# Kernel tuning notes

Measured on AMD Instinct MI355X. Metric: run time of the kernel, lower is better.

## Reference

```python
import jax, jax.numpy as jnp
import numpy as np


def _patchify(x, p):
    # x: [B, V, H, W] -> [B, V, L, p*p] with L = (H/p)*(W/p), matching Conv2d(kernel=stride=p)
    B, V, H, W = x.shape
    hp, wp = H // p, W // p
    x = x.reshape(B, V, hp, p, wp, p)
    x = x.transpose(0, 1, 2, 4, 3, 5)  # [B, V, hp, wp, p, p]
    return x.reshape(B, V, hp * wp, p * p)


def setup_inputs() -> dict:
    key = jax.random.key(0)
    ks = jax.random.split(key, 12)
    B, V, H, W, p, D = 2, 16, 128, 256, 4, 1024
    L = (H // p) * (W // p)  # 2048
    std = 0.02
    return {
        "x": jax.random.normal(ks[0], (B, V, H, W), jnp.float32),
        "proj_w": jax.random.normal(ks[1], (V, D, p * p), jnp.float32) * std,
        "proj_b": jnp.zeros((V, D), jnp.float32),
        "channel_embed": jax.random.normal(ks[2], (1, V, D), jnp.float32) * std,
        "pos_embed": jax.random.normal(ks[3], (1, L, D), jnp.float32) * std,
        "channel_query": jax.random.normal(ks[4], (1, 1, D), jnp.float32) * std,
        "wq": jax.random.normal(ks[5], (D, D), jnp.float32) * std,
        "wk": jax.random.normal(ks[6], (D, D), jnp.float32) * std,
        "wv": jax.random.normal(ks[7], (D, D), jnp.float32) * std,
        "bq": jnp.zeros((D,), jnp.float32),
        "bk": jnp.zeros((D,), jnp.float32),
        "bv": jnp.zeros((D,), jnp.float32),
        "wo": jax.random.normal(ks[8], (D, D), jnp.float32) * std,
        "bo": jnp.zeros((D,), jnp.float32),
        "num_heads": 16,
    }


def reference(x, proj_w, proj_b, channel_embed, pos_embed, channel_query,
              wq, wk, wv, bq, bk, bv, wo, bo, num_heads):
    D = proj_w.shape[1]
    p = int(round(np.sqrt(proj_w.shape[-1])))
    nh = int(num_heads)
    dh = D // nh

    # per-variable patch embed (Conv2d k=stride=p == patch-matmul)
    patches = _patchify(x, p)                                   # [B, V, L, p*p]
    tok = jnp.einsum('bvlk,vdk->bvld', patches, proj_w)         # [B, V, L, D]
    tok = tok + proj_b[None, :, None, :]

    # add variable (channel) and positional embeddings
    tok = tok + channel_embed[:, :, None, :] + pos_embed[:, None, :, :]

    # aggregate_variables: single-query MHA over V, batched over B*L
    h = tok.transpose(0, 2, 1, 3)                               # [B, L, V, D]
    q = channel_query[0, 0] @ wq.T + bq                         # [D]
    qh = q.reshape(nh, dh)
    k = (jnp.einsum('blvd,ed->blve', h, wk) + bk).reshape(*h.shape[:3], nh, dh)
    v = (jnp.einsum('blvd,ed->blve', h, wv) + bv).reshape(*h.shape[:3], nh, dh)
    scores = jnp.einsum('he,blvhe->blhv', qh, k) / np.sqrt(dh)  # [B, L, nh, V]
    attn = jax.nn.softmax(scores, axis=-1)
    ctx = jnp.einsum('blhv,blvhe->blhe', attn, v)               # [B, L, nh, dh]
    ctx = ctx.reshape(h.shape[0], h.shape[1], D)
    out = ctx @ wo.T + bo                                       # [B, L, D]
    return out
```

## Files before the change

kernel.cpp:

```cpp
#include <hip/hip_runtime.h>
#include <hip/hip_bf16.h>

using bf16 = __hip_bfloat16;
using bf16x8 = __attribute__((ext_vector_type(8))) short;
using f32x4  = __attribute__((ext_vector_type(4))) float;

__device__ inline unsigned short f2bu(float f){ bf16 h = __float2bfloat16(f); return *(unsigned short*)&h; }
__device__ inline void async_cp16(const void* g, void* l){
  __builtin_amdgcn_global_load_lds((const __attribute__((address_space(1))) void*)g,
                                   (__attribute__((address_space(3))) void*)l, 16, 0, 0);
}
union BF8 { unsigned short s[8]; bf16x8 v; };

constexpr int D_ = 1024, L_ = 2048;
constexpr int CN = 384;

__device__ inline size_t w3idx(int row, int col){
  const int hh = row >> 6, m = row & 15, dt = (row >> 4) & 3;
  const int vp = col >> 5, quad = (col >> 3) & 3, j = col & 7;
  return (size_t)hh*18432 + vp*2048 + dt*512 + quad*128 + m*8 + j;
}

__global__ __launch_bounds__(256) void k_prep2(const float* __restrict__ wv, const float* __restrict__ wo,
                                               const float* __restrict__ pe,
                                               const float* __restrict__ proj_w, const float* __restrict__ proj_b,
                                               const float* __restrict__ ce, const float* __restrict__ cq,
                                               const float* __restrict__ wq, const float* __restrict__ bq,
                                               const float* __restrict__ wk,
                                               unsigned short* __restrict__ Ab, unsigned short* __restrict__ wo_b,
                                               unsigned short* __restrict__ pe_b,
                                               unsigned short* __restrict__ Btb){
  __shared__ float t[64][17];
  __shared__ float qL[64];
  __shared__ float red[4][64];
  const int blk = blockIdx.x;
  const int tid = threadIdx.x;
  if (blk < 4096){
    int i = blk*256 + tid;
    const float* src; unsigned short* dst; size_t off;
    if (i < 262144){ src = wv; dst = Ab;   off = i; }
    else if (i < 524288){ src = wo; dst = wo_b; off = i - 262144; }
    else           { src = pe; dst = pe_b; off = i - 524288; }
    float4 v = *(const float4*)(src + off*4);
    *(ushort4*)(dst + off*4) = make_ushort4(f2bu(v.x), f2bu(v.y), f2bu(v.z), f2bu(v.w));
  } else if (blk < 4352){
    const int r_ = blk - 4096;
    const int v = r_ >> 4, dd0 = (r_ & 15)*64;
    { const int r = tid >> 2, kq = tid & 3;
      float4 a = *(const float4*)(proj_w + ((size_t)(v*D_ + dd0 + r))*16 + kq*4);
      t[r][kq*4+0]=a.x; t[r][kq*4+1]=a.y; t[r][kq*4+2]=a.z; t[r][kq*4+3]=a.w; }
    __syncthreads();
    { const int k = tid >> 4, c0 = (tid & 15)*4;
      ushort4 o = make_ushort4(f2bu(t[c0+0][k]), f2bu(t[c0+1][k]), f2bu(t[c0+2][k]), f2bu(t[c0+3][k]));
      *(ushort4*)(Btb + (size_t)(v*16+k)*D_ + dd0 + c0) = o; }
    if (tid < 16){
      const int c0 = tid*4;
      float4 pb = *(const float4*)(proj_b + v*D_ + dd0 + c0);
      float4 cc = *(const float4*)(ce     + v*D_ + dd0 + c0);
      ushort4 o = make_ushort4(f2bu(pb.x+cc.x), f2bu(pb.y+cc.y), f2bu(pb.z+cc.z), f2bu(pb.w+cc.w));
      *(ushort4*)(Btb + (size_t)(256+v)*D_ + dd0 + c0) = o;
    }
  } else {
    const int b = blk - 4352;
    const int hh = b >> 4, dq = b & 15;
    const int wave = tid >> 6, lane = tid & 63;
    {
      float cqv[16];
      #pragma unroll
      for (int k=0;k<16;++k) cqv[k] = cq[lane + 64*k];
      #pragma unroll
      for (int j=0;j<16;++j){
        const int e = hh*64 + wave*16 + j;
        const float* wr = wq + (size_t)e*D_;
        float p = 0.f;
        #pragma unroll
        for (int k=0;k<16;++k) p += cqv[k]*wr[lane + 64*k];
        #pragma unroll
        for (int m=32;m>=1;m>>=1) p += __shfl_xor(p, m, 64);
        if (lane==0) qL[wave*16+j] = p + bq[e];
      }
    }
    __syncthreads();
    {
      const int eg = wave, dl = lane;
      const int d = dq*64 + dl;
      float s = 0.f;
      #pragma unroll
      for (int j=0;j<16;++j){
        int e = hh*64 + eg*16 + j;
        s += qL[eg*16+j]*wk[(size_t)e*D_ + d];
      }
      red[eg][dl] = s;
      __syncthreads();
      if (eg==0)
        Ab[(size_t)(1024+hh)*D_ + d] = f2bu(((red[0][dl]+red[1][dl]) + (red[2][dl]+red[3][dl]))*0.125f);
    }
  }
}

template<int MFRAG, bool BIAS, bool WB2>
__device__ inline void gemm_body(unsigned short* As, unsigned short* Bs,
                                 const unsigned short* __restrict__ Abf, const unsigned short* __restrict__ Bt,
                                 const float* __restrict__ bias, float* __restrict__ C,
                                 unsigned short* __restrict__ W, const float* __restrict__ bvp,
                                 int m0, int n0, int K, int ldc, int Mvalid){
  const int tid = threadIdx.x;
  const int wave = tid >> 6, lane = tid & 63;
  const int wm = wave & 1, wn = wave >> 1;
  const int lm = lane & 15, kg4 = lane >> 4;
  f32x4 acc[MFRAG][4];
  #pragma unroll
  for (int mf=0;mf<MFRAG;++mf)
    #pragma unroll
    for (int nf=0;nf<4;++nf) acc[mf][nf] = (f32x4){0.f,0.f,0.f,0.f};
  for (int k0=0; k0<K; k0+=64){
    #pragma unroll
    for (int i=0;i<MFRAG;++i){
      int idx = i*256 + tid;
      int row = idx >> 3, g = (idx & 7) ^ (row & 7);
      async_cp16(Abf + (size_t)(m0+row)*K + k0 + g*8, &As[idx*8]);
    }
    #pragma unroll
    for (int i=0;i<4;++i){
      int idx = i*256 + tid;
      int row = idx >> 3, g = (idx & 7) ^ (row & 7);
      async_cp16(Bt + (size_t)(n0+row)*K + k0 + g*8, &Bs[idx*8]);
    }
    __syncthreads();
    #pragma unroll
    for (int c=0;c<2;++c){
      bf16x8 af[MFRAG], bfr[4];
      #pragma unroll
      for (int f=0;f<MFRAG;++f){
        int row = wm*16*MFRAG + f*16 + lm;
        af[f] = *(const bf16x8*)(&As[row*64 + (((c*4+kg4) ^ (row&7)))*8]);
      }
      #pragma unroll
      for (int f=0;f<4;++f){
        int colr = wn*64 + f*16 + lm;
        bfr[f] = *(const bf16x8*)(&Bs[colr*64 + (((c*4+kg4) ^ (colr&7)))*8]);
      }
      #pragma unroll
      for (int mf=0;mf<MFRAG;++mf)
        #pragma unroll
        for (int nf=0;nf<4;++nf)
          acc[mf][nf] = __builtin_amdgcn_mfma_f32_16x16x32_bf16(af[mf], bfr[nf], acc[mf][nf], 0,0,0);
    }
    __syncthreads();
  }
  #pragma unroll
  for (int nf=0;nf<4;++nf){
    int col = n0 + wn*64 + nf*16 + lm;
    float bval = BIAS ? bias[col] : 0.f;
    #pragma unroll
    for (int mf=0;mf<MFRAG;++mf){
      #pragma unroll
      for (int r=0;r<4;++r){
        int row = m0 + wm*16*MFRAG + mf*16 + kg4*4 + r;
        if (row < Mvalid){
          float v = acc[mf][nf][r];
          C[(size_t)row*ldc + col] = v + bval;
          if (WB2 && row < 1024){
            if (col < 256)      W[w3idx(row,col)] = f2bu(v);
            else if (col < 272) W[w3idx(row,col)] = f2bu(v + bvp[row]);
            else if (col < 288) W[w3idx(row,col)] = 0;
          }
        }
      }
    }
  }
}

__global__ __launch_bounds__(256) void k_gemmCP2(const unsigned short* __restrict__ Ab,
                                                 const unsigned short* __restrict__ Btb,
                                                 const unsigned short* __restrict__ pe_b,
                                                 const float* __restrict__ bv,
                                                 float* __restrict__ Cbig, unsigned short* __restrict__ Wb2,
                                                 float* __restrict__ P2){
  __shared__ unsigned short As[64*64];
  __shared__ unsigned short Bs[128*64];
  if (blockIdx.x < 51){
    int bx = blockIdx.x % 3, by = blockIdx.x / 3;
    gemm_body<2,false,true>(As, Bs, Ab, Btb, nullptr, Cbig, Wb2, bv, by*64, bx*128, 1024, CN, 1040);
  } else {
    int b = blockIdx.x - 51;
    int bx = b & 7, by = b >> 3;
    gemm_body<1,false,false>(As, Bs, pe_b, Ab, nullptr, P2, nullptr, nullptr, by*32, bx*128, 1024, 1024, 2048);
  }
}

__global__ __launch_bounds__(256) void k_gemmOut(const unsigned short* __restrict__ ctxF,
                                                 const unsigned short* __restrict__ wo_b,
                                                 const float* __restrict__ bo, float* __restrict__ C){
  __shared__ unsigned short As[64*64];
  __shared__ unsigned short Bs[128*64];
  gemm_body<2,true,false>(As, Bs, ctxF, wo_b, bo, C, nullptr, nullptr,
                          blockIdx.y*64, blockIdx.x*128, 1024, 1024, 4096);
}

__global__ __launch_bounds__(1024) void k_fused10(const float* __restrict__ x,
                                                  const float* __restrict__ Cbig,
                                                  const unsigned short* __restrict__ W3,
                                                  const float* __restrict__ P2,
                                                  unsigned short* __restrict__ ctxF){
  __shared__ float patchP[16*260];
  __shared__ float attnT[16*320];
  __shared__ __align__(16) unsigned short S[16*1032];
  const int tid = threadIdx.x;
  const int bb  = blockIdx.x >> 7;
  const int sg  = blockIdx.x & 127;
  unsigned short* ctx = ctxF + (size_t)bb*L_*D_;
  const int l0 = sg*16;
  {
    const int u = tid & 15, pi = (tid >> 4) & 3, v = tid >> 6;
    const int hi = l0 >> 6, wi0 = l0 & 63;
    const float* xp = x + ((size_t)((bb*16+v)*128 + hi*4 + pi)*256 + (wi0+u)*4);
    float4 r = *(const float4*)xp;
    float* dst = &patchP[u*260 + v*16 + pi*4];
    dst[0]=r.x; dst[1]=r.y; dst[2]=r.z; dst[3]=r.w;
  }
  __syncthreads();
  if (tid < 256){
    const int s = tid >> 4, h = tid & 15;
    const float* qrow = Cbig + (size_t)(1024+h)*CN;
    const float* prow = &patchP[s*260];
    float4 qc0 = *(const float4*)(qrow+256);
    float4 qc1 = *(const float4*)(qrow+260);
    float4 qc2 = *(const float4*)(qrow+264);
    float4 qc3 = *(const float4*)(qrow+268);
    float qcv[16] = {qc0.x,qc0.y,qc0.z,qc0.w, qc1.x,qc1.y,qc1.z,qc1.w,
                     qc2.x,qc2.y,qc2.z,qc2.w, qc3.x,qc3.y,qc3.z,qc3.w};
    float sc[16];
    #pragma unroll
    for (int v=0; v<16; ++v){
      const float* qp = qrow + v*16;
      const float* pp = prow + v*16;
      float4 qa = *(const float4*)(qp+0),  qb = *(const float4*)(qp+4);
      float4 qc = *(const float4*)(qp+8),  qd = *(const float4*)(qp+12);
      float4 pa = *(const float4*)(pp+0),  pb2 = *(const float4*)(pp+4);
      float4 pc = *(const float4*)(pp+8),  pd = *(const float4*)(pp+12);
      float a = qcv[v];
      a += qa.x*pa.x + qa.y*pa.y + qa.z*pa.z + qa.w*pa.w;
      a += qb.x*pb2.x + qb.y*pb2.y + qb.z*pb2.z + qb.w*pb2.w;
      a += qc.x*pc.x + qc.y*pc.y + qc.z*pc.z + qc.w*pc.w;
      a += qd.x*pd.x + qd.y*pd.y + qd.z*pd.z + qd.w*pd.w;
      sc[v] = a;
    }
    float mx = sc[0];
    #pragma unroll
    for (int v=1;v<16;++v) mx = fmaxf(mx, sc[v]);
    float sum = 0.f;
    #pragma unroll
    for (int v=0;v<16;++v){ sc[v] = __expf(sc[v]-mx); sum += sc[v]; }
    float inv = 1.f/sum;
    float* arow = &attnT[h*320 + s*20];
    #pragma unroll
    for (int v=0;v<16;++v) arow[v] = sc[v]*inv;
  }
  __syncthreads();
  const int wave = tid >> 6, lane = tid & 63;
  const int m = lane & 15, quad = lane >> 4;
  const int hh = wave;
  const float* at = &attnT[hh*320];
  const unsigned short* wbase = W3 + (size_t)hh*18432 + lane*8;
  f32x4 acc[4];
  #pragma unroll
  for (int dt=0;dt<4;++dt) acc[dt] = (f32x4){0.f,0.f,0.f,0.f};
  #pragma unroll
  for (int vp=0; vp<9; ++vp){
    BF8 af;
    if (vp < 8){
      const int v = vp*2 + (quad>>1);
      const int k8 = (quad&1)*8;
      const float aw = at[m*20 + v];
      const float* pp = &patchP[m*260 + v*16 + k8];
      float4 p0 = *(const float4*)(pp+0);
      float4 p1 = *(const float4*)(pp+4);
      af.s[0]=f2bu(aw*p0.x); af.s[1]=f2bu(aw*p0.y); af.s[2]=f2bu(aw*p0.z); af.s[3]=f2bu(aw*p0.w);
      af.s[4]=f2bu(aw*p1.x); af.s[5]=f2bu(aw*p1.y); af.s[6]=f2bu(aw*p1.z); af.s[7]=f2bu(aw*p1.w);
    } else {
      #pragma unroll
      for (int j=0;j<8;++j)
        af.s[j] = (quad < 2) ? f2bu(at[m*20 + quad*8 + j]) : (unsigned short)0;
    }
    #pragma unroll
    for (int dt=0; dt<4; ++dt){
      const bf16x8 bf = *(const bf16x8*)(wbase + vp*2048 + dt*512);
      acc[dt] = __builtin_amdgcn_mfma_f32_16x16x32_bf16(af.v, bf, acc[dt], 0,0,0);
    }
  }
  #pragma unroll
  for (int dt=0; dt<4; ++dt){
    const int d = hh*64 + dt*16 + m;
    #pragma unroll
    for (int r=0;r<4;++r){
      const int s = quad*4 + r;
      S[s*1032 + d] = f2bu(acc[dt][r] + P2[(size_t)(l0+s)*D_ + d]);
    }
  }
  __syncthreads();
  {
    const int row = tid >> 6, ch = tid & 63;
    const unsigned short* srcp = &S[row*1032 + ch*16];
    unsigned short* dstp = ctx + (size_t)(l0+row)*D_ + ch*16;
    *(uint4*)(dstp)   = *(const uint4*)(srcp);
    *(uint4*)(dstp+8) = *(const uint4*)(srcp+8);
  }
}

extern "C" void kernel_launch(void* const* d_in, const int* in_sizes, int n_in,
                              void* d_out, int out_size, void* d_ws, size_t ws_size,
                              hipStream_t stream){
  const float* x      = (const float*)d_in[0];
  const float* proj_w = (const float*)d_in[1];
  const float* proj_b = (const float*)d_in[2];
  const float* ce     = (const float*)d_in[3];
  const float* pe     = (const float*)d_in[4];
  const float* cq     = (const float*)d_in[5];
  const float* wq     = (const float*)d_in[6];
  const float* wk     = (const float*)d_in[7];
  const float* wv     = (const float*)d_in[8];
  const float* bq     = (const float*)d_in[9];
  const float* bv     = (const float*)d_in[11];
  const float* wo     = (const float*)d_in[12];
  const float* bo     = (const float*)d_in[13];
  float* out = (float*)d_out;

  char* base = (char*)d_ws;
  unsigned short* Ab   = (unsigned short*)(base);
  unsigned short* Btb  = (unsigned short*)(base + 2359296);
  float*          Cbig = (float*)(base + 3145728);
  unsigned short* wo_b = (unsigned short*)(base + 4743168);
  unsigned short* Wb2  = (unsigned short*)(base + 6840320);
  float*          P2   = (float*)(base + 7430144);
  unsigned short* ctxF = (unsigned short*)(base + 15818752);
  unsigned short* pe_b = (unsigned short*)(base + 24207360);

  k_prep2<<<4608, 256, 0, stream>>>(wv, wo, pe, proj_w, proj_b, ce, cq, wq, bq, wk, Ab, wo_b, pe_b, Btb);
  k_gemmCP2<<<563, 256, 0, stream>>>(Ab, Btb, pe_b, bv, Cbig, Wb2, P2);
  k_fused10<<<256, 1024, 0, stream>>>(x, Cbig, Wb2, P2, ctxF);
  k_gemmOut<<<dim3(8,64), 256, 0, stream>>>(ctxF, wo_b, bo, out);
}
```

Baseline: 172.1 us.

## Move pos-embed × Wv GEMM into prep kernel, reading fp32 inputs directly

The P2 = pos_embed·Wvᵀ GEMM moves from the second kernel into the prep kernel. It loads fp32 pe and wv and converts them to bf16 while filling LDS, which removes the pe_b buffer and its separate conversion pass. The qK projection is also restructured from 16 column blocks per head to one block per head. The second kernel now runs only the 51 Cbig tiles. The trade-off is a simpler, non-async-copy GEMM loop inside prep, with no double buffering and fp32 global loads that are twice as wide.

```diff
diff --git a/kernel.cpp b/kernel.cpp
--- a/kernel.cpp
+++ b/kernel.cpp
@@ -21,30 +21,28 @@
   return (size_t)hh*18432 + vp*2048 + dt*512 + quad*128 + m*8 + j;
 }
 
-__global__ __launch_bounds__(256) void k_prep2(const float* __restrict__ wv, const float* __restrict__ wo,
-                                               const float* __restrict__ pe,
-                                               const float* __restrict__ proj_w, const float* __restrict__ proj_b,
-                                               const float* __restrict__ ce, const float* __restrict__ cq,
-                                               const float* __restrict__ wq, const float* __restrict__ bq,
-                                               const float* __restrict__ wk,
-                                               unsigned short* __restrict__ Ab, unsigned short* __restrict__ wo_b,
-                                               unsigned short* __restrict__ pe_b,
-                                               unsigned short* __restrict__ Btb){
-  __shared__ float t[64][17];
-  __shared__ float qL[64];
-  __shared__ float red[4][64];
+__global__ __launch_bounds__(256) void k_prepP2(const float* __restrict__ wv, const float* __restrict__ wo,
+                                                const float* __restrict__ pe,
+                                                const float* __restrict__ proj_w, const float* __restrict__ proj_b,
+                                                const float* __restrict__ ce, const float* __restrict__ cq,
+                                                const float* __restrict__ wq, const float* __restrict__ bq,
+                                                const float* __restrict__ wk,
+                                                unsigned short* __restrict__ Ab, unsigned short* __restrict__ wo_b,
+                                                unsigned short* __restrict__ Btb,
+                                                float* __restrict__ P2){
+  __shared__ __align__(16) char smem[20480];
   const int blk = blockIdx.x;
   const int tid = threadIdx.x;
-  if (blk < 4096){
+  if (blk < 2048){
     int i = blk*256 + tid;
     const float* src; unsigned short* dst; size_t off;
     if (i < 262144){ src = wv; dst = Ab;   off = i; }
-    else if (i < 524288){ src = wo; dst = wo_b; off = i - 262144; }
-    else           { src = pe; dst = pe_b; off = i - 524288; }
+    else           { src = wo; dst = wo_b; off = i - 262144; }
     float4 v = *(const float4*)(src + off*4);
     *(ushort4*)(dst + off*4) = make_ushort4(f2bu(v.x), f2bu(v.y), f2bu(v.z), f2bu(v.w));
-  } else if (blk < 4352){
-    const int r_ = blk - 4096;
+  } else if (blk < 2304){
+    float (*t)[17] = (float(*)[17])smem;
+    const int r_ = blk - 2048;
     const int v = r_ >> 4, dd0 = (r_ & 15)*64;
     { const int r = tid >> 2, kq = tid & 3;
       float4 a = *(const float4*)(proj_w + ((size_t)(v*D_ + dd0 + r))*16 + kq*4);
@@ -60,9 +58,9 @@
       ushort4 o = make_ushort4(f2bu(pb.x+cc.x), f2bu(pb.y+cc.y), f2bu(pb.z+cc.z), f2bu(pb.w+cc.w));
       *(ushort4*)(Btb + (size_t)(256+v)*D_ + dd0 + c0) = o;
     }
-  } else {
-    const int b = blk - 4352;
-    const int hh = b >> 4, dq = b & 15;
+  } else if (blk < 2320){
+    float* qL = (float*)smem;
+    const int hh = blk - 2304;
     const int wave = tid >> 6, lane = tid & 63;
     {
       float cqv[16];
@@ -81,19 +79,74 @@
       }
     }
     __syncthreads();
-    {
-      const int eg = wave, dl = lane;
-      const int d = dq*64 + dl;
-      float s = 0.f;
-      #pragma unroll
-      for (int j=0;j<16;++j){
-        int e = hh*64 + eg*16 + j;
-        s += qL[eg*16+j]*wk[(size_t)e*D_ + d];
-      }
-      red[eg][dl] = s;
+    #pragma unroll
+    for (int dd=0; dd<4; ++dd){
+      const int d = dd*256 + tid;
+      float s0=0.f, s1=0.f, s2=0.f, s3=0.f;
+      #pragma unroll
+      for (int j=0;j<16;++j) s0 += qL[j]    * wk[(size_t)(hh*64      + j)*D_ + d];
+      #pragma unroll
+      for (int j=0;j<16;++j) s1 += qL[16+j] * wk[(size_t)(hh*64 + 16 + j)*D_ + d];
+      #pragma unroll
+      for (int j=0;j<16;++j) s2 += qL[32+j] * wk[(size_t)(hh*64 + 32 + j)*D_ + d];
+      #pragma unroll
+      for (int j=0;j<16;++j) s3 += qL[48+j] * wk[(size_t)(hh*64 + 48 + j)*D_ + d];
+      Ab[(size_t)(1024+hh)*D_ + d] = f2bu(((s0+s1)+(s2+s3))*0.125f);
+    }
+  } else {
+    unsigned short* As = (unsigned short*)smem;
+    unsigned short* Bs = (unsigned short*)(smem + 4096);
+    const int b = blk - 2320;
+    const int bx = b & 7, by = b >> 3;
+    const int m0 = by*32, n0 = bx*128;
+    const int wave = tid >> 6, lane = tid & 63;
+    const int wm = wave & 1, wn = wave >> 1;
+    const int lm = lane & 15, kg4 = lane >> 4;
+    f32x4 acc[4];
+    #pragma unroll
+    for (int nf=0;nf<4;++nf) acc[nf] = (f32x4){0.f,0.f,0.f,0.f};
+    for (int k0=0; k0<1024; k0+=64){
+      { int idx = tid;
+        int row = idx >> 3, g = (idx & 7) ^ (row & 7);
+        const float* gp = pe + (size_t)(m0+row)*D_ + k0 + g*8;
+        float4 a0 = *(const float4*)gp, a1 = *(const float4*)(gp+4);
+        *(ushort4*)(&As[idx*8])   = make_ushort4(f2bu(a0.x),f2bu(a0.y),f2bu(a0.z),f2bu(a0.w));
+        *(ushort4*)(&As[idx*8+4]) = make_ushort4(f2bu(a1.x),f2bu(a1.y),f2bu(a1.z),f2bu(a1.w));
+      }
+      #pragma unroll
+      for (int i=0;i<4;++i){
+        int idx = i*256 + tid;
+        int row = idx >> 3, g = (idx & 7) ^ (row & 7);
+        const float* gp = wv + (size_t)(n0+row)*D_ + k0 + g*8;
+        float4 b0 = *(const float4*)gp, b1 = *(const float4*)(gp+4);
+        *(ushort4*)(&Bs[idx*8])   = make_ushort4(f2bu(b0.x),f2bu(b0.y),f2bu(b0.z),f2bu(b0.w));
+        *(ushort4*)(&Bs[idx*8+4]) = make_ushort4(f2bu(b1.x),f2bu(b1.y),f2bu(b1.z),f2bu(b1.w));
+      }
       __syncthreads();
-      if (eg==0)
-        Ab[(size_t)(1024+hh)*D_ + d] = f2bu(((red[0][dl]+red[1][dl]) + (red[2][dl]+red[3][dl]))*0.125f);
+      #pragma unroll
+      for (int c=0;c<2;++c){
+        bf16x8 af, bfr[4];
+        { int row = wm*16 + lm;
+          af = *(const bf16x8*)(&As[row*64 + (((c*4+kg4) ^ (row&7)))*8]); }
+        #pragma unroll
+        for (int f=0;f<4;++f){
+          int colr = wn*64 + f*16 + lm;
+          bfr[f] = *(const bf16x8*)(&Bs[colr*64 + (((c*4+kg4) ^ (colr&7)))*8]);
+        }
+        #pragma unroll
+        for (int nf=0;nf<4;++nf)
+          acc[nf] = __builtin_amdgcn_mfma_f32_16x16x32_bf16(af, bfr[nf], acc[nf], 0,0,0);
+      }
+      __syncthreads();
+    }
+    #pragma unroll
+    for (int nf=0;nf<4;++nf){
+      int col = n0 + wn*64 + nf*16 + lm;
+      #pragma unroll
+      for (int r=0;r<4;++r){
+        int row = m0 + wm*16 + kg4*4 + r;
+        P2[(size_t)row*D_ + col] = acc[nf][r];
+      }
     }
   }
 }
@@ -171,22 +224,14 @@
   }
 }
 
-__global__ __launch_bounds__(256) void k_gemmCP2(const unsigned short* __restrict__ Ab,
-                                                 const unsigned short* __restrict__ Btb,
-                                                 const unsigned short* __restrict__ pe_b,
-                                                 const float* __restrict__ bv,
-                                                 float* __restrict__ Cbig, unsigned short* __restrict__ Wb2,
-                                                 float* __restrict__ P2){
+__global__ __launch_bounds__(256) void k_gemmCbig(const unsigned short* __restrict__ Ab,
+                                                  const unsigned short* __restrict__ Btb,
+                                                  const float* __restrict__ bv,
+                                                  float* __restrict__ Cbig, unsigned short* __restrict__ Wb2){
   __shared__ unsigned short As[64*64];
   __shared__ unsigned short Bs[128*64];
-  if (blockIdx.x < 51){
-    int bx = blockIdx.x % 3, by = blockIdx.x / 3;
-    gemm_body<2,false,true>(As, Bs, Ab, Btb, nullptr, Cbig, Wb2, bv, by*64, bx*128, 1024, CN, 1040);
-  } else {
-    int b = blockIdx.x - 51;
-    int bx = b & 7, by = b >> 3;
-    gemm_body<1,false,false>(As, Bs, pe_b, Ab, nullptr, P2, nullptr, nullptr, by*32, bx*128, 1024, 1024, 2048);
-  }
+  int bx = blockIdx.x % 3, by = blockIdx.x / 3;
+  gemm_body<2,false,true>(As, Bs, Ab, Btb, nullptr, Cbig, Wb2, bv, by*64, bx*128, 1024, CN, 1040);
 }
 
 __global__ __launch_bounds__(256) void k_gemmOut(const unsigned short* __restrict__ ctxF,
@@ -334,10 +379,9 @@
   unsigned short* Wb2  = (unsigned short*)(base + 6840320);
   float*          P2   = (float*)(base + 7430144);
   unsigned short* ctxF = (unsigned short*)(base + 15818752);
-  unsigned short* pe_b = (unsigned short*)(base + 24207360);
-
-  k_prep2<<<4608, 256, 0, stream>>>(wv, wo, pe, proj_w, proj_b, ce, cq, wq, bq, wk, Ab, wo_b, pe_b, Btb);
-  k_gemmCP2<<<563, 256, 0, stream>>>(Ab, Btb, pe_b, bv, Cbig, Wb2, P2);
+
+  k_prepP2<<<2832, 256, 0, stream>>>(wv, wo, pe, proj_w, proj_b, ce, cq, wq, bq, wk, Ab, wo_b, Btb, P2);
+  k_gemmCbig<<<51, 256, 0, stream>>>(Ab, Btb, bv, Cbig, Wb2);
   k_fused10<<<256, 1024, 0, stream>>>(x, Cbig, Wb2, P2, ctxF);
   k_gemmOut<<<dim3(8,64), 256, 0, stream>>>(ctxF, wo_b, bo, out);
 }
```

Result: slower. 189.3 us (+10.0%).
